# Performance work log

Measured on AMD Instinct MI355X. Metric: run time of the kernel, lower is better.

Reference implementation:

```python
import jax, jax.numpy as jnp
import numpy as np

SIGMA = 1.0
SQRT2 = float(np.sqrt(2.0))


def setup_inputs() -> dict:
    key = jax.random.key(0)
    k1, k2 = jax.random.split(key)
    B, L = 128, 1024
    preds = jax.random.normal(k1, (B, L), dtype=jnp.float32)
    # integer relevance grades 0..4, stored as float as in the torch module
    target = jax.random.randint(k2, (B, L), 0, 5).astype(jnp.float32)
    return {"preds": preds, "target": target}


def reference(preds, target):
    B, L = preds.shape
    # pairwise diff [B, L, L]: diff[b,i,j] = preds[b,i] - preds[b,j]
    diff = preds[:, :, None] - preds[:, None, :]
    # Normal(0, sigma*sqrt(2)).cdf(diff) == ndtr(diff / (sigma*sqrt(2)))
    p = jax.scipy.special.ndtr(diff / (SIGMA * SQRT2))
    # zero the diagonal (i == j) before summing
    eye = jnp.eye(L, dtype=bool)
    p = jnp.where(eye[None, :, :], 0.0, p)
    expected_ranks = 1.0 + p.sum(axis=2)  # [B, L]

    gains = 2.0 ** target - 1.0
    discounts = jnp.log2(expected_ranks + 1.0)
    dcg = (gains / discounts).sum(axis=1)  # [B]

    ideal_target = jnp.sort(target, axis=1)[:, ::-1]  # descending
    ideal_gains = 2.0 ** ideal_target - 1.0
    ideal_discounts = jnp.log2(jnp.arange(1, L + 1, dtype=jnp.float32) + 1.0)
    idcg = (ideal_gains / ideal_discounts).sum(axis=1)  # [B]

    ndcg = dcg / (idcg + 1e-10)
    return -ndcg.mean()
```

## Files before the change

kernel.cpp:

```cpp
#include <hip/hip_runtime.h>

#define B 128
#define L 1024


#if __has_builtin(__builtin_amdgcn_exp2f)
#define EXP2(x) __builtin_amdgcn_exp2f(x)
#else
#define EXP2(x) __expf((x) * 0.6931471805599453f)
#endif

__device__ __forceinline__ float phi_sigmoid(float z) {
    float z2 = z * z;
    float q  = __builtin_fmaf(z2, -0.10179656f, -2.3048496f);
    float w  = z * q;
    float e  = EXP2(w);
    return __builtin_amdgcn_rcpf(1.0f + e);
}

__global__ __launch_bounds__(256) void pair_kernel(const float* __restrict__ preds,
                                                   const float* __restrict__ target,
                                                   float* __restrict__ ws) {
    __shared__ float sp[L];

    const int b    = blockIdx.x >> 2;
    const int iseg = blockIdx.x & 3;
    const int tid  = threadIdx.x;
    const float* row = preds + b * L;

    if (blockIdx.x == 0 && tid == 0) {
        ws[2048] = 0.0f;
        ((int*)ws)[2049] = 0;
    }

    float4 v4 = reinterpret_cast<const float4*>(row)[tid];
    const float inv_sqrt2 = 0.70710678118654752f;
    v4.x *= inv_sqrt2; v4.y *= inv_sqrt2; v4.z *= inv_sqrt2; v4.w *= inv_sqrt2;
    reinterpret_cast<float4*>(sp)[tid] = v4;

    const int i = iseg * 256 + tid;
    float tgt = target[b * L + i];

    __syncthreads();

    const float pi = sp[i];

    float s0 = 0.0f, s1 = 0.0f, s2 = 0.0f, s3 = 0.0f;
    #pragma unroll 4
    for (int j = 0; j < L; j += 4) {
        float4 v = *reinterpret_cast<const float4*>(&sp[j]);
        s0 += phi_sigmoid(pi - v.x);
        s1 += phi_sigmoid(pi - v.y);
        s2 += phi_sigmoid(pi - v.z);
        s3 += phi_sigmoid(pi - v.w);
    }
    float s = (s0 + s1) + (s2 + s3);
    float er1 = 1.5f + s;

    float g = EXP2(tgt) - 1.0f;
    float contrib = g * __builtin_amdgcn_rcpf(__log2f(er1));

    #pragma unroll
    for (int off = 32; off > 0; off >>= 1)
        contrib += __shfl_down(contrib, off);
    if ((tid & 63) == 0)
        ws[b * 16 + iseg * 4 + (tid >> 6)] = contrib;
}

__global__ __launch_bounds__(256) void finish_kernel(const float* __restrict__ target,
                                                     float* __restrict__ ws,
                                                     float* __restrict__ out) {
    __shared__ unsigned long long cred[256];
    __shared__ float2 fred[256];

    const int b   = blockIdx.x;
    const int tid = threadIdx.x;
    const float* row = target + b * L;

    unsigned long long cnt = 0ull;
    #pragma unroll
    for (int k = 0; k < 4; ++k) {
        float t = row[tid + k * 256];
        cnt += ((unsigned long long)(t > 3.5f) << 48)
             + ((unsigned long long)(t > 2.5f) << 32)
             + ((unsigned long long)(t > 1.5f) << 16)
             + ((unsigned long long)(t > 0.5f));
    }
    cred[tid] = cnt;
    __syncthreads();
    #pragma unroll
    for (int s = 128; s > 0; s >>= 1) {
        if (tid < (unsigned)s) cred[tid] += cred[tid + s];
        __syncthreads();
    }
    unsigned long long tot = cred[0];
    const int n4 = (int)(tot >> 48) & 0xFFFF;
    const int n3 = (int)(tot >> 32) & 0xFFFF;
    const int n2 = (int)(tot >> 16) & 0xFFFF;
    const int n1 = (int)(tot)       & 0xFFFF;

    float idcg_p = 0.0f;
    #pragma unroll
    for (int k = 0; k < 4; ++k) {
        int pos = tid + 1 + k * 256;
        float gain = (pos <= n4) ? 15.0f : (pos <= n3) ? 7.0f :
                     (pos <= n2) ? 3.0f  : (pos <= n1) ? 1.0f : 0.0f;
        idcg_p += gain * __builtin_amdgcn_rcpf(__log2f((float)pos + 1.0f));
    }
    float dcg_p = (tid < 16) ? ws[b * 16 + tid] : 0.0f;
    fred[tid] = make_float2(idcg_p, dcg_p);
    __syncthreads();
    #pragma unroll
    for (int s = 128; s > 0; s >>= 1) {
        if (tid < (unsigned)s) {
            float2 a = fred[tid], c = fred[tid + s];
            fred[tid] = make_float2(a.x + c.x, a.y + c.y);
        }
        __syncthreads();
    }

    if (tid == 0) {
        float ndcg = fred[0].y / (fred[0].x + 1e-10f);
        atomicAdd(&ws[2048], ndcg);
        __threadfence();
        int old = atomicAdd((int*)ws + 2049, 1);
        if (old == B - 1) {
            float acc = atomicAdd(&ws[2048], 0.0f);
            out[0] = -acc * (1.0f / (float)B);
        }
    }
}

extern "C" void kernel_launch(void* const* d_in, const int* in_sizes, int n_in,
                              void* d_out, int out_size, void* d_ws, size_t ws_size,
                              hipStream_t stream) {
    const float* preds  = (const float*)d_in[0];
    const float* target = (const float*)d_in[1];
    float* out = (float*)d_out;
    float* ws  = (float*)d_ws;

    pair_kernel<<<B * 4, 256, 0, stream>>>(preds, target, ws);
    finish_kernel<<<B, 256, 0, stream>>>(target, ws, out);
}
```

Baseline: 96.85 us.

## Use antisymmetric erf approximation and fuse finish into pair kernel via last-block

Replaces the sigmoid-style Phi approximation with an odd erf-like form (copysign of 1 minus an exp2 of a cubic in |d|). Summing these terms gives the rank sum via 0.5*E plus a constant, and the diagonal term is zero by construction. The separate finish kernel is folded into the pair kernel: the last block per row, detected with an atomic counter, computes IDCG and the ndcg. A small init kernel zeroes the workspace. This removes a dependent launch and shortens per-pair arithmetic, but adds atomics and a new approximation whose accuracy may differ.

```diff
diff --git a/kernel.cpp b/kernel.cpp
--- a/kernel.cpp
+++ b/kernel.cpp
@@ -2,7 +2,6 @@
 
 #define B 128
 #define L 1024
-
 
 #if __has_builtin(__builtin_amdgcn_exp2f)
 #define EXP2(x) __builtin_amdgcn_exp2f(x)
@@ -10,52 +9,69 @@
 #define EXP2(x) __expf((x) * 0.6931471805599453f)
 #endif
 
-__device__ __forceinline__ float phi_sigmoid(float z) {
-    float z2 = z * z;
-    float q  = __builtin_fmaf(z2, -0.10179656f, -2.3048496f);
-    float w  = z * q;
-    float e  = EXP2(w);
-    return __builtin_amdgcn_rcpf(1.0f + e);
+
+__global__ __launch_bounds__(256) void init_ws(float* ws) {
+    int t = threadIdx.x;
+    ws[t] = 0.0f;
+    if (t < 2) ws[256 + t] = 0.0f;
 }
 
-__global__ __launch_bounds__(256) void pair_kernel(const float* __restrict__ preds,
-                                                   const float* __restrict__ target,
-                                                   float* __restrict__ ws) {
+#define K1 -1.6279072f
+#define K2 -0.9299637f
+#define K3 -0.1074808f
+
+__device__ __forceinline__ float phi_term(float pi, float pj) {
+    float d = pi - pj;
+    float a = __builtin_fabsf(d);
+    float t = __builtin_fmaf(K3, a, K2);
+    float u = __builtin_fmaf(t, a, K1);
+    float e = EXP2(a * u);
+    return __builtin_copysignf(1.0f - e, d);
+}
+
+__global__ __launch_bounds__(256) void pair_fused_kernel(const float* __restrict__ preds,
+                                                         const float* __restrict__ target,
+                                                         float* __restrict__ ws,
+                                                         float* __restrict__ out) {
     __shared__ float sp[L];
+    __shared__ float wred[4];
+    __shared__ int lastflag;
+    __shared__ unsigned long long cred[256];
+    __shared__ float fred[256];
 
     const int b    = blockIdx.x >> 2;
     const int iseg = blockIdx.x & 3;
     const int tid  = threadIdx.x;
-    const float* row = preds + b * L;
+    const float* prow = preds + b * L;
+    const float* trow = target + b * L;
 
-    if (blockIdx.x == 0 && tid == 0) {
-        ws[2048] = 0.0f;
-        ((int*)ws)[2049] = 0;
-    }
-
-    float4 v4 = reinterpret_cast<const float4*>(row)[tid];
-    const float inv_sqrt2 = 0.70710678118654752f;
-    v4.x *= inv_sqrt2; v4.y *= inv_sqrt2; v4.z *= inv_sqrt2; v4.w *= inv_sqrt2;
+    float4 v4 = reinterpret_cast<const float4*>(prow)[tid];
+    v4.x *= 0.5f; v4.y *= 0.5f; v4.z *= 0.5f; v4.w *= 0.5f;
     reinterpret_cast<float4*>(sp)[tid] = v4;
 
     const int i = iseg * 256 + tid;
-    float tgt = target[b * L + i];
+    const float tgt = trow[i];
 
     __syncthreads();
 
     const float pi = sp[i];
 
-    float s0 = 0.0f, s1 = 0.0f, s2 = 0.0f, s3 = 0.0f;
-    #pragma unroll 4
-    for (int j = 0; j < L; j += 4) {
-        float4 v = *reinterpret_cast<const float4*>(&sp[j]);
-        s0 += phi_sigmoid(pi - v.x);
-        s1 += phi_sigmoid(pi - v.y);
-        s2 += phi_sigmoid(pi - v.z);
-        s3 += phi_sigmoid(pi - v.w);
+    float a0 = 0.f, a1 = 0.f, a2 = 0.f, a3 = 0.f,
+          a4 = 0.f, a5 = 0.f, a6 = 0.f, a7 = 0.f;
+    for (int j = 0; j < L; j += 8) {
+        float4 va = *reinterpret_cast<const float4*>(&sp[j]);
+        float4 vb = *reinterpret_cast<const float4*>(&sp[j + 4]);
+        a0 += phi_term(pi, va.x);
+        a1 += phi_term(pi, va.y);
+        a2 += phi_term(pi, va.z);
+        a3 += phi_term(pi, va.w);
+        a4 += phi_term(pi, vb.x);
+        a5 += phi_term(pi, vb.y);
+        a6 += phi_term(pi, vb.z);
+        a7 += phi_term(pi, vb.w);
     }
-    float s = (s0 + s1) + (s2 + s3);
-    float er1 = 1.5f + s;
+    float E = ((a0 + a1) + (a2 + a3)) + ((a4 + a5) + (a6 + a7));
+    float er1 = 513.5f + 0.5f * E;
 
     float g = EXP2(tgt) - 1.0f;
     float contrib = g * __builtin_amdgcn_rcpf(__log2f(er1));
@@ -63,24 +79,24 @@
     #pragma unroll
     for (int off = 32; off > 0; off >>= 1)
         contrib += __shfl_down(contrib, off);
-    if ((tid & 63) == 0)
-        ws[b * 16 + iseg * 4 + (tid >> 6)] = contrib;
-}
+    if ((tid & 63) == 0) wred[tid >> 6] = contrib;
+    __syncthreads();
 
-__global__ __launch_bounds__(256) void finish_kernel(const float* __restrict__ target,
-                                                     float* __restrict__ ws,
-                                                     float* __restrict__ out) {
-    __shared__ unsigned long long cred[256];
-    __shared__ float2 fred[256];
+    if (tid == 0) {
+        float blocksum = (wred[0] + wred[1]) + (wred[2] + wred[3]);
+        atomicAdd(&ws[b], blocksum);
+        __threadfence();
+        int old = atomicAdd((int*)ws + 128 + b, 1);
+        lastflag = (old == 3);
+    }
+    __syncthreads();
 
-    const int b   = blockIdx.x;
-    const int tid = threadIdx.x;
-    const float* row = target + b * L;
+    if (!lastflag) return;
 
     unsigned long long cnt = 0ull;
     #pragma unroll
     for (int k = 0; k < 4; ++k) {
-        float t = row[tid + k * 256];
+        float t = trow[tid + k * 256];
         cnt += ((unsigned long long)(t > 3.5f) << 48)
              + ((unsigned long long)(t > 2.5f) << 32)
              + ((unsigned long long)(t > 1.5f) << 16)
@@ -107,25 +123,23 @@
                      (pos <= n2) ? 3.0f  : (pos <= n1) ? 1.0f : 0.0f;
         idcg_p += gain * __builtin_amdgcn_rcpf(__log2f((float)pos + 1.0f));
     }
-    float dcg_p = (tid < 16) ? ws[b * 16 + tid] : 0.0f;
-    fred[tid] = make_float2(idcg_p, dcg_p);
+    fred[tid] = idcg_p;
     __syncthreads();
     #pragma unroll
     for (int s = 128; s > 0; s >>= 1) {
-        if (tid < (unsigned)s) {
-            float2 a = fred[tid], c = fred[tid + s];
-            fred[tid] = make_float2(a.x + c.x, a.y + c.y);
-        }
+        if (tid < (unsigned)s) fred[tid] += fred[tid + s];
         __syncthreads();
     }
 
     if (tid == 0) {
-        float ndcg = fred[0].y / (fred[0].x + 1e-10f);
-        atomicAdd(&ws[2048], ndcg);
         __threadfence();
-        int old = atomicAdd((int*)ws + 2049, 1);
-        if (old == B - 1) {
-            float acc = atomicAdd(&ws[2048], 0.0f);
+        float dcgv = atomicAdd(&ws[b], 0.0f);
+        float ndcg = dcgv / (fred[0] + 1e-10f);
+        atomicAdd(&ws[256], ndcg);
+        __threadfence();
+        int old2 = atomicAdd((int*)ws + 257, 1);
+        if (old2 == B - 1) {
+            float acc = atomicAdd(&ws[256], 0.0f);
             out[0] = -acc * (1.0f / (float)B);
         }
     }
@@ -139,6 +153,6 @@
     float* out = (float*)d_out;
     float* ws  = (float*)d_ws;
 
-    pair_kernel<<<B * 4, 256, 0, stream>>>(preds, target, ws);
-    finish_kernel<<<B, 256, 0, stream>>>(target, ws, out);
+    init_ws<<<1, 256, 0, stream>>>(ws);
+    pair_fused_kernel<<<B * 4, 256, 0, stream>>>(preds, target, ws, out);
 }
```

Result: no change. 95.67 us (-1.2%).
